# Kernel tuning notes

Measured on AMD Instinct MI355X. Metric: run time of the kernel, lower is better.

The kernel has to match this reference:

```python
import jax, jax.numpy as jnp
import numpy as np

B, N, R = 4, 16, 64        # batch, permuted axis size, inner spatial size
M, S = N // 2, R * 2       # block count, block size


def _glorot(key, shape):
    fan_in, fan_out = shape[-2], shape[-1]
    lim = np.sqrt(6.0 / (fan_in + fan_out)).astype(np.float32)
    return jax.random.uniform(key, shape, jnp.float32, -lim, lim)


def setup_inputs() -> dict:
    key = jax.random.key(0)
    ks = jax.random.split(key, 10)
    inp = {
        "x": jax.random.normal(ks[0], (B, N, R, N, R, 2), jnp.float32),
        "perm_idx": jax.random.permutation(ks[1], N).astype(jnp.int32),
    }
    for i, name in enumerate(["hr1", "hi1", "hr2", "hi2", "hr3", "hi3", "hr4", "hi4"]):
        inp[name] = _glorot(ks[2 + i], (M, S, S))
    return inp


def _bilin(v, p_right, p_left):
    # v: (B, m, s, m, s). First contract the last s-axis against p_right's
    # block matmuls (block index = axis 3), then the axis-2 s-axis against
    # p_left's block matmuls (block index = axis 1).
    t = jnp.einsum('bmiaj,ajk->bmiak', v, p_right)
    return jnp.einsum('xbjci,bjk->xbkci', t, p_left)


def reference(x, perm_idx, hr1, hi1, hr2, hi2, hr3, hi3, hr4, hi4):
    m = x.shape[1] // 2
    s = x.shape[2] * 2
    n, r = m * 2, s // 2
    x = x.take(perm_idx, axis=1).take(perm_idx, axis=3)
    x = x.reshape((-1, m, s, m, s, 2))
    x_re, x_im = x[..., 0], x[..., 1]

    y_re = (_bilin(x_re, hr1, hr1) + _bilin(x_re, hi1, hi1)
            + _bilin(x_im, hi2, hr2) + _bilin(x_im, hr2, hi2))
    y_im = (_bilin(x_im, hr3, hr3) + _bilin(x_im, hi3, hi3)
            + _bilin(x_re, hi4, hr4) + _bilin(x_re, hr4, hi4))

    y = jnp.stack([y_re, y_im], axis=-1)
    return y.reshape((-1, n, r, n, r, 2))
```

## Files before the change

kernel.cpp:

```cpp
#include <hip/hip_runtime.h>
#include <hip/hip_bf16.h>
#include <stdint.h>

typedef __attribute__((ext_vector_type(8))) short bf16x8;
typedef __attribute__((ext_vector_type(4))) float f32x4;
typedef __attribute__((ext_vector_type(16))) float f32x16;

#define MFMA32(a, b, c) __builtin_amdgcn_mfma_f32_32x32x16_bf16((a), (b), (c), 0, 0, 0)

__device__ __forceinline__ unsigned short f2bf_rn(float f) {
    union { __bf16 b; unsigned short u; } v;
    v.b = (__bf16)f;
    return v.u;
}

__device__ __forceinline__ unsigned int pk2(float lo, float hi) {
    union { unsigned short s[2]; unsigned int u; } r;
    r.s[0] = f2bf_rn(lo); r.s[1] = f2bf_rn(hi);
    return r.u;
}

__device__ __forceinline__ void gload_lds16(const void* g, void* l) {
    __builtin_amdgcn_global_load_lds(
        (const __attribute__((address_space(1))) void*)g,
        (__attribute__((address_space(3))) void*)l, 16, 0, 0);
}

__global__ __launch_bounds__(256) void prep_h(
    const float* __restrict__ h0, const float* __restrict__ h1,
    const float* __restrict__ h2, const float* __restrict__ h3,
    const float* __restrict__ h4, const float* __restrict__ h5,
    const float* __restrict__ h6, const float* __restrict__ h7,
    unsigned short* __restrict__ ht)
{
    const float* hmap[8] = {h0, h1, h2, h3, h4, h5, h6, h7};
    const int wg = blockIdx.x;
    const float* src = hmap[wg >> 3] + (wg & 7) * 16384;
    unsigned short* dst = ht + wg * 16384;
    __shared__ unsigned short tile[128 * 129];
    const int t = threadIdx.x;
    #pragma unroll 4
    for (int i = 0; i < 64; ++i) {
        int idx = t + 256 * i, r = idx >> 7, k = idx & 127;
        tile[r * 129 + k] = f2bf_rn(src[idx]);
    }
    __syncthreads();
    #pragma unroll 4
    for (int i = 0; i < 64; ++i) {
        int idx = t + 256 * i, k = idx >> 7, r = idx & 127;
        dst[idx] = tile[r * 129 + k];
    }
}

__global__ __launch_bounds__(512, 2) void bilin_main(
    const float* __restrict__ x, const int* __restrict__ perm,
    const unsigned short* __restrict__ ht, float* __restrict__ out)
{
    const int wg = blockIdx.x;
    const int q = wg & 7, p = (wg >> 3) & 7, b = wg >> 6;
    const int tid = threadIdx.x;
    const int lane = tid & 63, wid = tid >> 6;
    const int wn = wid & 3, h = wid >> 2;
    const int l31 = lane & 31, hl = lane >> 5;

    __shared__ __align__(16) unsigned short smem[81920];
    unsigned short* xre_lds = smem;
    unsigned short* xim_lds = smem + 16384;
    unsigned short* llds = smem + 65536;

    constexpr int cseq[8]  = {0, 1, 6, 7, 2, 3, 4, 5};
    constexpr int rperm[8] = {0, 1, 3, 2, 4, 5, 7, 6};

    const int wubase = tid & ~63;
    auto stage_h = [&](unsigned short* dst, int blk) {
        const unsigned short* src = ht + blk * 16384;
        #pragma unroll
        for (int r = 0; r < 4; ++r) {
            const int idx = r * 512 + tid;
            const int row = idx >> 4, cin = idx & 15;
            gload_lds16(src + row * 128 + ((cin ^ (row & 15)) << 3),
                        dst + ((r * 512 + wubase) << 3));
        }
    };

    auto ldr = [&](const unsigned short* base, int row, int ch) -> bf16x8 {
        return *(const bf16x8*)(base + row * 128 + ((ch ^ (row & 15)) << 3));
    };

    float4 xv[4][4];
    int woffs[4];
    #pragma unroll
    for (int i = 0; i < 4; ++i) {
        const int idx = i * 512 + tid;
        const int row = idx >> 4, cin = idx & 15;
        const int n1 = perm[2 * p + (row >> 6)];
        const int n2 = perm[2 * q + (cin >> 3)];
        const int r1 = row & 63, r2 = (cin & 7) * 8;
        const float* sp = x + ((size_t)((b * 16 + n1) * 64 + r1) * 1024
                               + n2 * 64 + r2) * 2;
        #pragma unroll
        for (int j = 0; j < 4; ++j)
            xv[i][j] = *(const float4*)(sp + j * 4);
        woffs[i] = row * 128 + ((cin ^ (row & 15)) << 3);
    }
    stage_h(smem + 32768, rperm[0] * 8 + q);
    stage_h(llds, 0 * 8 + p);
    #pragma unroll
    for (int i = 0; i < 4; ++i) {
        bf16x8 re, im;
        #pragma unroll
        for (int j = 0; j < 4; ++j) {
            re[2 * j]     = (short)f2bf_rn(xv[i][j].x);
            re[2 * j + 1] = (short)f2bf_rn(xv[i][j].z);
            im[2 * j]     = (short)f2bf_rn(xv[i][j].y);
            im[2 * j + 1] = (short)f2bf_rn(xv[i][j].w);
        }
        *(bf16x8*)(xre_lds + woffs[i]) = re;
        *(bf16x8*)(xim_lds + woffs[i]) = im;
    }
    __syncthreads();

    f32x16 yre[4], yim[4];
    #pragma unroll
    for (int i = 0; i < 4; ++i) {
        #pragma unroll
        for (int e = 0; e < 16; ++e) { yre[i][e] = 0.f; yim[i][e] = 0.f; }
    }

    #pragma unroll
    for (int cc = 0; cc < 8; ++cc) {
        const unsigned short* wb = smem + 32768 + (cc & 1) * 16384;
        const unsigned short* xg = (cc < 4) ? xre_lds : xim_lds;

        f32x16 u[2];
        #pragma unroll
        for (int e = 0; e < 16; ++e) { u[0][e] = 0.f; u[1][e] = 0.f; }
        #pragma unroll
        for (int ks = 0; ks < 8; ++ks) {
            bf16x8 wfr = ldr(wb, wn * 32 + l31, 2 * ks + hl);
            #pragma unroll
            for (int m2 = 0; m2 < 2; ++m2) {
                bf16x8 xfr = ldr(xg, h * 64 + m2 * 32 + l31, 2 * ks + hl);
                u[m2] = MFMA32(xfr, wfr, u[m2]);
            }
        }

        __syncthreads();
        if (cc < 7)
            stage_h(smem + 32768 + ((cc + 1) & 1) * 16384,
                    rperm[cseq[cc + 1]] * 8 + q);

        #pragma unroll
        for (int t = 0; t < 4; ++t) {
            const int f = t >> 1, qa = (t & 1) * 2, qb = qa + 1;
            unsigned int lo0 = pk2(u[f][4 * qa + 0], u[f][4 * qa + 1]);
            unsigned int lo1 = pk2(u[f][4 * qa + 2], u[f][4 * qa + 3]);
            unsigned int hi0 = pk2(u[f][4 * qb + 0], u[f][4 * qb + 1]);
            unsigned int hi1 = pk2(u[f][4 * qb + 2], u[f][4 * qb + 3]);
            unsigned int sxl0 = (unsigned int)__shfl_xor((int)lo0, 32);
            unsigned int sxl1 = (unsigned int)__shfl_xor((int)lo1, 32);
            unsigned int sxh0 = (unsigned int)__shfl_xor((int)hi0, 32);
            unsigned int sxh1 = (unsigned int)__shfl_xor((int)hi1, 32);
            union { unsigned int d[4]; bf16x8 v; } ufu;
            ufu.d[0] = hl ? sxh0 : lo0;
            ufu.d[1] = hl ? sxh1 : lo1;
            ufu.d[2] = hl ? hi0 : sxl0;
            ufu.d[3] = hl ? hi1 : sxl1;
            #pragma unroll
            for (int mt = 0; mt < 4; ++mt) {
                bf16x8 lfr = ldr(llds, mt * 32 + l31, 8 * h + 2 * t + hl);
                if ((cc & 3) < 2) yre[mt] = MFMA32(lfr, ufu.v, yre[mt]);
                else              yim[mt] = MFMA32(lfr, ufu.v, yim[mt]);
            }
        }

        __syncthreads();
        if (cc < 7)
            stage_h(llds, cseq[cc + 1] * 8 + p);
    }

    float* red = (float*)smem + wn * 8192;
    if (h == 1) {
        #pragma unroll
        for (int mt = 0; mt < 4; ++mt)
            #pragma unroll
            for (int q4 = 0; q4 < 4; ++q4) {
                f32x4 vr, vi;
                #pragma unroll
                for (int jj = 0; jj < 4; ++jj) {
                    vr[jj] = yre[mt][4 * q4 + jj];
                    vi[jj] = yim[mt][4 * q4 + jj];
                }
                *(f32x4*)(red + ((0 * 4 + mt) * 4 + q4) * 256 + lane * 4) = vr;
                *(f32x4*)(red + ((1 * 4 + mt) * 4 + q4) * 256 + lane * 4) = vi;
            }
    }
    __syncthreads();
    if (h == 0) {
        float2* o2 = (float2*)out;
        #pragma unroll
        for (int mt = 0; mt < 4; ++mt)
            #pragma unroll
            for (int q4 = 0; q4 < 4; ++q4) {
                f32x4 pr = *(const f32x4*)(red + ((0 * 4 + mt) * 4 + q4) * 256 + lane * 4);
                f32x4 pi = *(const f32x4*)(red + ((1 * 4 + mt) * 4 + q4) * 256 + lane * 4);
                #pragma unroll
                for (int jj = 0; jj < 4; ++jj) {
                    const int j = 4 * q4 + jj;
                    const int row = mt * 32 + (j & 3) + 8 * (j >> 2) + 4 * hl;
                    float2 v;
                    v.x = yre[mt][j] + pr[jj];
                    v.y = yim[mt][j] + pi[jj];
                    o2[(size_t)(b * 1024 + p * 128 + row) * 1024
                       + q * 128 + wn * 32 + l31] = v;
                }
            }
    }
}

extern "C" void kernel_launch(void* const* d_in, const int* in_sizes, int n_in,
                              void* d_out, int out_size, void* d_ws, size_t ws_size,
                              hipStream_t stream) {
    const float* x  = (const float*)d_in[0];
    const int* perm = (const int*)d_in[1];
    unsigned short* htp = (unsigned short*)d_ws;

    hipLaunchKernelGGL(prep_h, dim3(64), dim3(256), 0, stream,
        (const float*)d_in[2], (const float*)d_in[3], (const float*)d_in[4],
        (const float*)d_in[5], (const float*)d_in[6], (const float*)d_in[7],
        (const float*)d_in[8], (const float*)d_in[9], htp);
    hipLaunchKernelGGL(bilin_main, dim3(256), dim3(512), 0, stream,
        x, perm, htp, (float*)d_out);
}
```

Before: 42.48 us.

## Double-buffer both weight stages, stage x halves lazily, split transpose prep

The main kernel now double-buffers both the right and left weight blocks and issues the next iteration's async global-to-LDS loads at the start of each iteration. This cuts the per-iteration barriers from two to one. To free LDS for this, only one of the real/imaginary x planes is kept at a time, and the imaginary plane is reloaded from global memory after iteration 3. The cross-half lane shuffle is trimmed from four to two shuffles. The prep transpose kernel is split across 4x more workgroups with smaller tiles. The cost is a second global read of x and an extra barrier at the midpoint.

```diff
diff --git a/kernel.cpp b/kernel.cpp
--- a/kernel.cpp
+++ b/kernel.cpp
@@ -35,20 +35,23 @@
 {
     const float* hmap[8] = {h0, h1, h2, h3, h4, h5, h6, h7};
     const int wg = blockIdx.x;
-    const float* src = hmap[wg >> 3] + (wg & 7) * 16384;
-    unsigned short* dst = ht + wg * 16384;
-    __shared__ unsigned short tile[128 * 129];
+    const int jblk = wg >> 2, qt = wg & 3;
+    const float* src = hmap[jblk >> 3] + (jblk & 7) * 16384;
+    unsigned short* dst = ht + jblk * 16384;
+    __shared__ unsigned short tile[32 * 129];
     const int t = threadIdx.x;
-    #pragma unroll 4
-    for (int i = 0; i < 64; ++i) {
-        int idx = t + 256 * i, r = idx >> 7, k = idx & 127;
-        tile[r * 129 + k] = f2bf_rn(src[idx]);
+    #pragma unroll
+    for (int i = 0; i < 16; ++i) {
+        int idx = t + 256 * i;
+        int r = idx >> 5, kk = idx & 31;
+        tile[kk * 129 + r] = f2bf_rn(src[r * 128 + qt * 32 + kk]);
     }
     __syncthreads();
-    #pragma unroll 4
-    for (int i = 0; i < 64; ++i) {
-        int idx = t + 256 * i, k = idx >> 7, r = idx & 127;
-        dst[idx] = tile[r * 129 + k];
+    #pragma unroll
+    for (int i = 0; i < 16; ++i) {
+        int idx = t + 256 * i;
+        int k = idx >> 7, r = idx & 127;
+        dst[(qt * 32 + k) * 128 + r] = tile[k * 129 + r];
     }
 }
 
@@ -64,12 +67,13 @@
     const int l31 = lane & 31, hl = lane >> 5;
 
     __shared__ __align__(16) unsigned short smem[81920];
-    unsigned short* xre_lds = smem;
-    unsigned short* xim_lds = smem + 16384;
-    unsigned short* llds = smem + 65536;
+    unsigned short* xlds = smem;
 
     constexpr int cseq[8]  = {0, 1, 6, 7, 2, 3, 4, 5};
     constexpr int rperm[8] = {0, 1, 3, 2, 4, 5, 7, 6};
+
+    const int n1a = perm[2 * p], n1b = perm[2 * p + 1];
+    const int n2a = perm[2 * q], n2b = perm[2 * q + 1];
 
     const int wubase = tid & ~63;
     auto stage_h = [&](unsigned short* dst, int blk) {
@@ -83,54 +87,67 @@
         }
     };
 
+    auto stage_x = [&](int g) {
+        float4 xv[4][4];
+        int woffs[4];
+        #pragma unroll
+        for (int i = 0; i < 4; ++i) {
+            const int idx = i * 512 + tid;
+            const int row = idx >> 4, cin = idx & 15;
+            const int n1 = (i >> 1) ? n1b : n1a;
+            const int n2 = (cin >> 3) ? n2b : n2a;
+            const int r1 = row & 63, r2 = (cin & 7) * 8;
+            const float* sp = x + ((size_t)((b * 16 + n1) * 64 + r1) * 1024
+                                   + n2 * 64 + r2) * 2;
+            #pragma unroll
+            for (int j = 0; j < 4; ++j)
+                xv[i][j] = *(const float4*)(sp + j * 4);
+            woffs[i] = row * 128 + ((cin ^ (row & 15)) << 3);
+        }
+        #pragma unroll
+        for (int i = 0; i < 4; ++i) {
+            bf16x8 t;
+            #pragma unroll
+            for (int j = 0; j < 4; ++j) {
+                if (g == 0) {
+                    t[2 * j]     = (short)f2bf_rn(xv[i][j].x);
+                    t[2 * j + 1] = (short)f2bf_rn(xv[i][j].z);
+                } else {
+                    t[2 * j]     = (short)f2bf_rn(xv[i][j].y);
+                    t[2 * j + 1] = (short)f2bf_rn(xv[i][j].w);
+                }
+            }
+            *(bf16x8*)(xlds + woffs[i]) = t;
+        }
+    };
+
     auto ldr = [&](const unsigned short* base, int row, int ch) -> bf16x8 {
         return *(const bf16x8*)(base + row * 128 + ((ch ^ (row & 15)) << 3));
     };
 
-    float4 xv[4][4];
-    int woffs[4];
+    stage_h(smem + 16384, rperm[0] * 8 + q);
+    stage_h(smem + 49152, 0 * 8 + p);
+    stage_x(0);
+    __syncthreads();
+
+    f32x16 yre[4], yim[4];
     #pragma unroll
     for (int i = 0; i < 4; ++i) {
-        const int idx = i * 512 + tid;
-        const int row = idx >> 4, cin = idx & 15;
-        const int n1 = perm[2 * p + (row >> 6)];
-        const int n2 = perm[2 * q + (cin >> 3)];
-        const int r1 = row & 63, r2 = (cin & 7) * 8;
-        const float* sp = x + ((size_t)((b * 16 + n1) * 64 + r1) * 1024
-                               + n2 * 64 + r2) * 2;
-        #pragma unroll
-        for (int j = 0; j < 4; ++j)
-            xv[i][j] = *(const float4*)(sp + j * 4);
-        woffs[i] = row * 128 + ((cin ^ (row & 15)) << 3);
-    }
-    stage_h(smem + 32768, rperm[0] * 8 + q);
-    stage_h(llds, 0 * 8 + p);
-    #pragma unroll
-    for (int i = 0; i < 4; ++i) {
-        bf16x8 re, im;
-        #pragma unroll
-        for (int j = 0; j < 4; ++j) {
-            re[2 * j]     = (short)f2bf_rn(xv[i][j].x);
-            re[2 * j + 1] = (short)f2bf_rn(xv[i][j].z);
-            im[2 * j]     = (short)f2bf_rn(xv[i][j].y);
-            im[2 * j + 1] = (short)f2bf_rn(xv[i][j].w);
-        }
-        *(bf16x8*)(xre_lds + woffs[i]) = re;
-        *(bf16x8*)(xim_lds + woffs[i]) = im;
-    }
-    __syncthreads();
-
-    f32x16 yre[4], yim[4];
-    #pragma unroll
-    for (int i = 0; i < 4; ++i) {
         #pragma unroll
         for (int e = 0; e < 16; ++e) { yre[i][e] = 0.f; yim[i][e] = 0.f; }
     }
 
     #pragma unroll
     for (int cc = 0; cc < 8; ++cc) {
-        const unsigned short* wb = smem + 32768 + (cc & 1) * 16384;
-        const unsigned short* xg = (cc < 4) ? xre_lds : xim_lds;
+        const unsigned short* wb = smem + 16384 + (cc & 1) * 16384;
+        const unsigned short* lb = smem + 49152 + (cc & 1) * 16384;
+
+        if (cc < 7) {
+            stage_h(smem + 16384 + ((cc + 1) & 1) * 16384,
+                    rperm[cseq[cc + 1]] * 8 + q);
+            stage_h(smem + 49152 + ((cc + 1) & 1) * 16384,
+                    cseq[cc + 1] * 8 + p);
+        }
 
         f32x16 u[2];
         #pragma unroll
@@ -140,15 +157,10 @@
             bf16x8 wfr = ldr(wb, wn * 32 + l31, 2 * ks + hl);
             #pragma unroll
             for (int m2 = 0; m2 < 2; ++m2) {
-                bf16x8 xfr = ldr(xg, h * 64 + m2 * 32 + l31, 2 * ks + hl);
+                bf16x8 xfr = ldr(xlds, h * 64 + m2 * 32 + l31, 2 * ks + hl);
                 u[m2] = MFMA32(xfr, wfr, u[m2]);
             }
         }
-
-        __syncthreads();
-        if (cc < 7)
-            stage_h(smem + 32768 + ((cc + 1) & 1) * 16384,
-                    rperm[cseq[cc + 1]] * 8 + q);
 
         #pragma unroll
         for (int t = 0; t < 4; ++t) {
@@ -157,26 +169,29 @@
             unsigned int lo1 = pk2(u[f][4 * qa + 2], u[f][4 * qa + 3]);
             unsigned int hi0 = pk2(u[f][4 * qb + 0], u[f][4 * qb + 1]);
             unsigned int hi1 = pk2(u[f][4 * qb + 2], u[f][4 * qb + 3]);
-            unsigned int sxl0 = (unsigned int)__shfl_xor((int)lo0, 32);
-            unsigned int sxl1 = (unsigned int)__shfl_xor((int)lo1, 32);
-            unsigned int sxh0 = (unsigned int)__shfl_xor((int)hi0, 32);
-            unsigned int sxh1 = (unsigned int)__shfl_xor((int)hi1, 32);
+            unsigned int send0 = hl ? lo0 : hi0;
+            unsigned int send1 = hl ? lo1 : hi1;
+            unsigned int sx0 = (unsigned int)__shfl_xor((int)send0, 32);
+            unsigned int sx1 = (unsigned int)__shfl_xor((int)send1, 32);
             union { unsigned int d[4]; bf16x8 v; } ufu;
-            ufu.d[0] = hl ? sxh0 : lo0;
-            ufu.d[1] = hl ? sxh1 : lo1;
-            ufu.d[2] = hl ? hi0 : sxl0;
-            ufu.d[3] = hl ? hi1 : sxl1;
+            ufu.d[0] = hl ? sx0 : lo0;
+            ufu.d[1] = hl ? sx1 : lo1;
+            ufu.d[2] = hl ? hi0 : sx0;
+            ufu.d[3] = hl ? hi1 : sx1;
             #pragma unroll
             for (int mt = 0; mt < 4; ++mt) {
-                bf16x8 lfr = ldr(llds, mt * 32 + l31, 8 * h + 2 * t + hl);
+                bf16x8 lfr = ldr(lb, mt * 32 + l31, 8 * h + 2 * t + hl);
                 if ((cc & 3) < 2) yre[mt] = MFMA32(lfr, ufu.v, yre[mt]);
                 else              yim[mt] = MFMA32(lfr, ufu.v, yim[mt]);
             }
         }
 
+        if (cc == 3) {
+            __syncthreads();
+            stage_x(1);
+        }
+
         __syncthreads();
-        if (cc < 7)
-            stage_h(llds, cseq[cc + 1] * 8 + p);
     }
 
     float* red = (float*)smem + wn * 8192;
@@ -225,7 +240,7 @@
     const int* perm = (const int*)d_in[1];
     unsigned short* htp = (unsigned short*)d_ws;
 
-    hipLaunchKernelGGL(prep_h, dim3(64), dim3(256), 0, stream,
+    hipLaunchKernelGGL(prep_h, dim3(256), dim3(256), 0, stream,
         (const float*)d_in[2], (const float*)d_in[3], (const float*)d_in[4],
         (const float*)d_in[5], (const float*)d_in[6], (const float*)d_in[7],
         (const float*)d_in[8], (const float*)d_in[9], htp);
```

Result: faster. 40.18 us (-5.4%).
